# Kernel tuning notes

Hardware: AMD Instinct MI355X
Metric: run time of the kernel (lower is better)

The kernel has to match this reference:

```python
import jax, jax.numpy as jnp
import numpy as np

B, H, G, N, D = 1, 32, 64, 128, 128   # batch, heads, blocks, block_len, head_dim
S = 256                               # sketch dim (multiple of 16)
BIT_PACK = 8


def setup_inputs() -> dict:
    key = jax.random.key(0)
    k1, k2, k3 = jax.random.split(key, 3)
    data = jax.random.normal(k1, (B, H, G, N, D), dtype=jnp.float32)
    # binary per-channel outlier mask, float {0,1}, shape matches data.shape[:3] + (D,)
    outlier_mask = jax.random.randint(k2, (B, H, G, D), 0, 2).astype(jnp.float32)
    # proj_dir_quant = proj_dir_score.T -> shape (S, D)
    proj_dir_quant = jax.random.normal(k3, (S, D), dtype=jnp.float32)
    return {"data": data, "outlier_mask": outlier_mask, "proj_dir_quant": proj_dir_quant}


def _pack_bits(sketch):
    # sketch: (..., S). Reshape to (..., S//8, 8), threshold at 0, pack sign bits into uint8.
    x = sketch.reshape(*sketch.shape[:-1], -1, BIT_PACK)
    enc = (2 ** jnp.arange(BIT_PACK, dtype=jnp.int32))  # [1,2,4,...,128]
    packed = ((x > 0).astype(jnp.int32) * enc).sum(axis=-1)  # max 255, fits uint8
    return packed.astype(jnp.uint8)


def reference(data, outlier_mask, proj_dir_quant):
    s = proj_dir_quant.shape[0]
    m = outlier_mask[..., None, :]                     # (B,H,G,1,D) broadcast over tokens
    key_outlier = data * m
    key_inlier = data * (1.0 - m)
    # '...nd,sd->...ns' : sign-random-projection sketch
    sk_outlier = jnp.einsum('bhgnd,sd->bhgns', key_outlier, proj_dir_quant)
    sk_inlier = jnp.einsum('bhgnd,sd->bhgns', key_inlier, proj_dir_quant)
    hash_inlier = _pack_bits(sk_inlier)                # (B,H,G,N,S//8)
    hash_outlier = _pack_bits(sk_outlier)[..., : s // 16]  # (B,H,G,N,S//16)
    return (hash_inlier, hash_outlier)
```

## Files before the change

### kernel.cpp

```cpp
#include <hip/hip_runtime.h>

#define NB_HG 2048
#define DIM_N 128
#define DIM_D 128
#define DIM_S 256
#define PH 32
#define BSW 128


__global__ void transpose_proj_kernel(const float* __restrict__ proj,
                                      float* __restrict__ projT)
{
    const int d = blockIdx.x;
    const int s = threadIdx.x;
    projT[d * DIM_S + s] = proj[s * DIM_D + d];
}

template<bool TP>
__global__ __launch_bounds__(256)
void qjl_sketch_kernel(const float* __restrict__ data,
                       const float* __restrict__ mask,
                       const float* __restrict__ pmat,
                       int* __restrict__ out)
{
    __shared__ float Xt[PH * DIM_N];
    __shared__ float Bs[PH * BSW];
    __shared__ int   cidx[DIM_D];
    __shared__ int   wcnt[2];

    const int type = blockIdx.x;
    const int hg   = blockIdx.y;
    const int tid  = threadIdx.x;

    bool sel = false; int pos = 0, w = 0;
    if (tid < 128) {
        const float m = mask[hg * DIM_D + tid];
        sel = (type == 2) ? (m != 0.0f) : (m == 0.0f);
        const unsigned long long bal = __ballot(sel);
        const int lane = tid & 63;
        w = tid >> 6;
        if (lane == 0) wcnt[w] = __popcll(bal);
        pos = __popcll(bal & ((1ull << lane) - 1ull));
    }
    __syncthreads();
    if (sel) cidx[pos + (w ? wcnt[0] : 0)] = tid;
    __syncthreads();
    const int K = wcnt[0] + wcnt[1];

    const int tn = tid & 15;
    const int ts = tid >> 4;
    const int C0 = 4 * tn;
    const int sl = ts * 8;
    const int sbase = (type == 1) ? 128 : 0;

    float acc[8][8];
    #pragma unroll
    for (int j = 0; j < 8; ++j)
        #pragma unroll
        for (int i = 0; i < 8; ++i) acc[j][i] = 0.0f;

    const int cl_s  = tid & 31;
    const int nh    = tid >> 5;
    const int pcs_s = 4 * (cl_s & 7);
    float* xrow = &Xt[cl_s * DIM_N];
    float* brow = &Bs[cl_s * BSW];

    float4 xr[4], br[4];

    auto LOADR = [&](int base, int kp) {
        if (cl_s < kp) {
            const int dg = cidx[base + cl_s];
            const float* Xs = data + (size_t)hg * (DIM_N * DIM_D) + dg;
            #pragma unroll
            for (int g = 0; g < 4; ++g) {
                const int n0 = nh * 16 + g * 4;
                xr[g].x = Xs[(size_t)(n0 + 0) * DIM_D];
                xr[g].y = Xs[(size_t)(n0 + 1) * DIM_D];
                xr[g].z = Xs[(size_t)(n0 + 2) * DIM_D];
                xr[g].w = Xs[(size_t)(n0 + 3) * DIM_D];
            }
            if (TP) {
                const float* Ps = pmat + (size_t)dg * DIM_S + sbase;
                #pragma unroll
                for (int g = 0; g < 4; ++g)
                    br[g] = *reinterpret_cast<const float4*>(Ps + nh * 16 + g * 4);
            } else {
                #pragma unroll
                for (int g = 0; g < 4; ++g) {
                    const int s0l = nh * 16 + g * 4;
                    br[g].x = pmat[(size_t)(sbase + s0l + 0) * DIM_D + dg];
                    br[g].y = pmat[(size_t)(sbase + s0l + 1) * DIM_D + dg];
                    br[g].z = pmat[(size_t)(sbase + s0l + 2) * DIM_D + dg];
                    br[g].w = pmat[(size_t)(sbase + s0l + 3) * DIM_D + dg];
                }
            }
        }
    };
    auto WRITER = [&](int kp) {
        if (cl_s < kp) {
            #pragma unroll
            for (int g = 0; g < 4; ++g) {
                const int n0 = nh * 16 + g * 4;
                *reinterpret_cast<float4*>(&xrow[n0 ^ pcs_s]) = xr[g];
                *reinterpret_cast<float4*>(&brow[n0 ^ pcs_s]) = br[g];
            }
        }
    };

    auto COMPUTE = [&](int kp) {
        #pragma unroll 8
        for (int cl = 0; cl < kp; ++cl) {
            const int pcs = 4 * (cl & 7);
            const int pA  = sl ^ pcs;
            const float4 bA = *reinterpret_cast<const float4*>(&Bs[cl * BSW + pA]);
            const float4 bB = *reinterpret_cast<const float4*>(&Bs[cl * BSW + (pA ^ 4)]);
            const int P = C0 ^ pcs;
            const float4 q0 = *reinterpret_cast<const float4*>(&Xt[cl * DIM_N + P]);
            const float4 q1 = *reinterpret_cast<const float4*>(&Xt[cl * DIM_N + P + 64]);
            const float bv[8] = {bA.x, bA.y, bA.z, bA.w, bB.x, bB.y, bB.z, bB.w};

            #pragma unroll
            for (int j = 0; j < 8; ++j) {
                acc[j][0] = fmaf(bv[j], q0.x, acc[j][0]);
                acc[j][1] = fmaf(bv[j], q0.y, acc[j][1]);
                acc[j][2] = fmaf(bv[j], q0.z, acc[j][2]);
                acc[j][3] = fmaf(bv[j], q0.w, acc[j][3]);
                acc[j][4] = fmaf(bv[j], q1.x, acc[j][4]);
                acc[j][5] = fmaf(bv[j], q1.y, acc[j][5]);
                acc[j][6] = fmaf(bv[j], q1.z, acc[j][6]);
                acc[j][7] = fmaf(bv[j], q1.w, acc[j][7]);
            }
        }
    };

    {
        const int kp0 = (K < PH) ? K : PH;
        LOADR(0, kp0);
        WRITER(kp0);
        __syncthreads();
    }
    for (int base = 0; base < K; base += PH) {
        const int kpc = (K - base < PH) ? (K - base) : PH;
        const int nb  = base + PH;
        const int kpn = (nb < K) ? ((K - nb < PH) ? (K - nb) : PH) : 0;
        if (kpn) LOADR(nb, kpn);
        COMPUTE(kpc);
        if (kpn) {
            __syncthreads();
            WRITER(kpn);
            __syncthreads();
        }
    }

    const size_t inl_total = (size_t)NB_HG * DIM_N * 32;
    #pragma unroll
    for (int i = 0; i < 8; ++i) {
        int byte = 0;
        #pragma unroll
        for (int j = 0; j < 8; ++j)
            if (acc[j][i] > 0.0f) byte |= (1 << j);
        const int n = (i < 4) ? (C0 + i) : (64 + C0 + (i - 4));
        size_t idx;
        if (type == 2)
            idx = inl_total + ((size_t)hg * DIM_N + n) * 16 + ts;
        else
            idx = ((size_t)hg * DIM_N + n) * 32 + (type == 1 ? 16 : 0) + ts;
        out[idx] = byte;
    }
}

extern "C" void kernel_launch(void* const* d_in, const int* in_sizes, int n_in,
                              void* d_out, int out_size, void* d_ws, size_t ws_size,
                              hipStream_t stream) {
    const float* data = (const float*)d_in[0];
    const float* mask = (const float*)d_in[1];
    const float* proj = (const float*)d_in[2];
    int* out = (int*)d_out;

    dim3 grid(3, NB_HG);
    const size_t tp_bytes = (size_t)DIM_D * DIM_S * sizeof(float);
    if (ws_size >= tp_bytes) {
        float* projT = (float*)d_ws;
        transpose_proj_kernel<<<DIM_D, DIM_S, 0, stream>>>(proj, projT);
        qjl_sketch_kernel<true><<<grid, 256, 0, stream>>>(data, mask, projT, out);
    } else {
        qjl_sketch_kernel<false><<<grid, 256, 0, stream>>>(data, mask, proj, out);
    }
}
```

Before: 215.6 us.

## Double-buffer shared-memory tiles with half-size chunks and a single barrier

Shared-memory staging tiles are split into two ping-pong buffers, and the per-iteration chunk of channels drops from 32 to 16. This removes one __syncthreads per iteration, because the next chunk is written into the alternate buffer while others may still read the current one. The cost is more loop iterations with smaller register prefetches, which gives less latency hiding per chunk. The FMA inner loop's bv array is also replaced with select expressions, which should compile to the same code.

```diff
diff --git a/kernel.cpp b/kernel.cpp
--- a/kernel.cpp
+++ b/kernel.cpp
@@ -4,7 +4,7 @@
 #define DIM_N 128
 #define DIM_D 128
 #define DIM_S 256
-#define PH 32
+#define PH 16
 #define BSW 128
 
 
@@ -23,8 +23,8 @@
                        const float* __restrict__ pmat,
                        int* __restrict__ out)
 {
-    __shared__ float Xt[PH * DIM_N];
-    __shared__ float Bs[PH * BSW];
+    __shared__ float Xt[2][PH * DIM_N];
+    __shared__ float Bs[2][PH * BSW];
     __shared__ int   cidx[DIM_D];
     __shared__ int   wcnt[2];
 
@@ -59,21 +59,19 @@
         #pragma unroll
         for (int i = 0; i < 8; ++i) acc[j][i] = 0.0f;
 
-    const int cl_s  = tid & 31;
-    const int nh    = tid >> 5;
+    const int cl_s  = tid & 15;
+    const int nh    = tid >> 4;
     const int pcs_s = 4 * (cl_s & 7);
-    float* xrow = &Xt[cl_s * DIM_N];
-    float* brow = &Bs[cl_s * BSW];
 
-    float4 xr[4], br[4];
+    float4 xr[2], br[2];
 
     auto LOADR = [&](int base, int kp) {
         if (cl_s < kp) {
             const int dg = cidx[base + cl_s];
             const float* Xs = data + (size_t)hg * (DIM_N * DIM_D) + dg;
             #pragma unroll
-            for (int g = 0; g < 4; ++g) {
-                const int n0 = nh * 16 + g * 4;
+            for (int g = 0; g < 2; ++g) {
+                const int n0 = nh * 8 + g * 4;
                 xr[g].x = Xs[(size_t)(n0 + 0) * DIM_D];
                 xr[g].y = Xs[(size_t)(n0 + 1) * DIM_D];
                 xr[g].z = Xs[(size_t)(n0 + 2) * DIM_D];
@@ -82,12 +80,12 @@
             if (TP) {
                 const float* Ps = pmat + (size_t)dg * DIM_S + sbase;
                 #pragma unroll
-                for (int g = 0; g < 4; ++g)
-                    br[g] = *reinterpret_cast<const float4*>(Ps + nh * 16 + g * 4);
+                for (int g = 0; g < 2; ++g)
+                    br[g] = *reinterpret_cast<const float4*>(Ps + nh * 8 + g * 4);
             } else {
                 #pragma unroll
-                for (int g = 0; g < 4; ++g) {
-                    const int s0l = nh * 16 + g * 4;
+                for (int g = 0; g < 2; ++g) {
+                    const int s0l = nh * 8 + g * 4;
                     br[g].x = pmat[(size_t)(sbase + s0l + 0) * DIM_D + dg];
                     br[g].y = pmat[(size_t)(sbase + s0l + 1) * DIM_D + dg];
                     br[g].z = pmat[(size_t)(sbase + s0l + 2) * DIM_D + dg];
@@ -96,39 +94,45 @@
             }
         }
     };
-    auto WRITER = [&](int kp) {
+    auto WRITER = [&](int b, int kp) {
         if (cl_s < kp) {
+            float* xrow = &Xt[b][cl_s * DIM_N];
+            float* brow = &Bs[b][cl_s * BSW];
             #pragma unroll
-            for (int g = 0; g < 4; ++g) {
-                const int n0 = nh * 16 + g * 4;
+            for (int g = 0; g < 2; ++g) {
+                const int n0 = nh * 8 + g * 4;
                 *reinterpret_cast<float4*>(&xrow[n0 ^ pcs_s]) = xr[g];
                 *reinterpret_cast<float4*>(&brow[n0 ^ pcs_s]) = br[g];
             }
         }
     };
 
-    auto COMPUTE = [&](int kp) {
+    auto COMPUTE = [&](int b, int kp) {
+        const float* Xb = Xt[b];
+        const float* Bb = Bs[b];
         #pragma unroll 8
         for (int cl = 0; cl < kp; ++cl) {
             const int pcs = 4 * (cl & 7);
             const int pA  = sl ^ pcs;
-            const float4 bA = *reinterpret_cast<const float4*>(&Bs[cl * BSW + pA]);
-            const float4 bB = *reinterpret_cast<const float4*>(&Bs[cl * BSW + (pA ^ 4)]);
+            const float4 bA = *reinterpret_cast<const float4*>(&Bb[cl * BSW + pA]);
+            const float4 bB = *reinterpret_cast<const float4*>(&Bb[cl * BSW + (pA ^ 4)]);
             const int P = C0 ^ pcs;
-            const float4 q0 = *reinterpret_cast<const float4*>(&Xt[cl * DIM_N + P]);
-            const float4 q1 = *reinterpret_cast<const float4*>(&Xt[cl * DIM_N + P + 64]);
-            const float bv[8] = {bA.x, bA.y, bA.z, bA.w, bB.x, bB.y, bB.z, bB.w};
+            const float4 q0 = *reinterpret_cast<const float4*>(&Xb[cl * DIM_N + P]);
+            const float4 q1 = *reinterpret_cast<const float4*>(&Xb[cl * DIM_N + P + 64]);
 
             #pragma unroll
             for (int j = 0; j < 8; ++j) {
-                acc[j][0] = fmaf(bv[j], q0.x, acc[j][0]);
-                acc[j][1] = fmaf(bv[j], q0.y, acc[j][1]);
-                acc[j][2] = fmaf(bv[j], q0.z, acc[j][2]);
-                acc[j][3] = fmaf(bv[j], q0.w, acc[j][3]);
-                acc[j][4] = fmaf(bv[j], q1.x, acc[j][4]);
-                acc[j][5] = fmaf(bv[j], q1.y, acc[j][5]);
-                acc[j][6] = fmaf(bv[j], q1.z, acc[j][6]);
-                acc[j][7] = fmaf(bv[j], q1.w, acc[j][7]);
+                const float bv = (j == 0) ? bA.x : (j == 1) ? bA.y : (j == 2) ? bA.z
+                               : (j == 3) ? bA.w : (j == 4) ? bB.x : (j == 5) ? bB.y
+                               : (j == 6) ? bB.z : bB.w;
+                acc[j][0] = fmaf(bv, q0.x, acc[j][0]);
+                acc[j][1] = fmaf(bv, q0.y, acc[j][1]);
+                acc[j][2] = fmaf(bv, q0.z, acc[j][2]);
+                acc[j][3] = fmaf(bv, q0.w, acc[j][3]);
+                acc[j][4] = fmaf(bv, q1.x, acc[j][4]);
+                acc[j][5] = fmaf(bv, q1.y, acc[j][5]);
+                acc[j][6] = fmaf(bv, q1.z, acc[j][6]);
+                acc[j][7] = fmaf(bv, q1.w, acc[j][7]);
             }
         }
     };
@@ -136,18 +140,18 @@
     {
         const int kp0 = (K < PH) ? K : PH;
         LOADR(0, kp0);
-        WRITER(kp0);
+        WRITER(0, kp0);
         __syncthreads();
     }
-    for (int base = 0; base < K; base += PH) {
+    int b = 0;
+    for (int base = 0; base < K; base += PH, b ^= 1) {
         const int kpc = (K - base < PH) ? (K - base) : PH;
         const int nb  = base + PH;
         const int kpn = (nb < K) ? ((K - nb < PH) ? (K - nb) : PH) : 0;
         if (kpn) LOADR(nb, kpn);
-        COMPUTE(kpc);
+        COMPUTE(b, kpc);
         if (kpn) {
-            __syncthreads();
-            WRITER(kpn);
+            WRITER(b ^ 1, kpn);
             __syncthreads();
         }
     }
```

Result: faster. 203.0 us (-5.9%).
